# Kernel optimization log

Measured on AMD Instinct MI355X. Metric: run time of the kernel, lower is better.

## Reference

```python
import jax, jax.numpy as jnp
import numpy as np

B, C, H, W, D, V = 1, 32, 128, 160, 48, 3


def _make_proj_matrices():
    # K @ [R|t] per view, small rotations/baselines so warps land mostly in-bounds
    K = np.array([[400.0, 0.0, 80.0], [0.0, 400.0, 64.0], [0.0, 0.0, 1.0]])
    mats = []
    for v in range(V):
        a = 0.04 * v
        R = np.array([[np.cos(a), 0.0, np.sin(a)], [0.0, 1.0, 0.0], [-np.sin(a), 0.0, np.cos(a)]])
        t = np.array([120.0 * v, 0.0, 0.0])  # baseline in mm, consistent with depth ~425..935
        P = np.eye(4)
        P[:3, :3] = K @ R
        P[:3, 3] = K @ t
        mats.append(P)
    return jnp.asarray(np.stack(mats)[None], dtype=jnp.float32)  # [1,V,4,4]


def setup_inputs() -> dict:
    key = jax.random.key(0)
    k0, k1, k2, kw = jax.random.split(key, 4)
    feat0 = jax.random.normal(k0, (B, C, H, W), jnp.float32)
    feat1 = jax.random.normal(k1, (B, C, H, W), jnp.float32)
    feat2 = jax.random.normal(k2, (B, C, H, W), jnp.float32)
    depth_values = jnp.broadcast_to(
        jnp.linspace(425.0, 935.0, D, dtype=jnp.float32)[None], (B, D))
    w_reg = jax.random.normal(kw, (1, C, 3, 3, 3), jnp.float32) * 0.05
    b_reg = jnp.zeros((1,), jnp.float32)
    return dict(feat0=feat0, feat1=feat1, feat2=feat2,
                proj_matrices=_make_proj_matrices(),
                depth_values=depth_values, w_reg=w_reg, b_reg=b_reg,
                num_depth=D)


def _bilinear_sample(fea, gx, gy):
    # fea: [C,H,W]; gx,gy: [N] pixel coords (align_corners=True convention),
    # zero padding outside image (matches F.grid_sample padding_mode='zeros').
    h, w = fea.shape[1], fea.shape[2]
    x0 = jnp.floor(gx)
    y0 = jnp.floor(gy)
    wx = gx - x0
    wy = gy - y0

    def corner(xi, yi, wgt):
        valid = ((xi >= 0) & (xi <= w - 1) & (yi >= 0) & (yi <= h - 1)).astype(fea.dtype)
        xc = jnp.clip(xi, 0, w - 1).astype(jnp.int32)
        yc = jnp.clip(yi, 0, h - 1).astype(jnp.int32)
        return fea[:, yc, xc] * (wgt * valid)[None]  # [C,N]

    return (corner(x0, y0, (1 - wx) * (1 - wy)) +
            corner(x0 + 1, y0, wx * (1 - wy)) +
            corner(x0, y0 + 1, (1 - wx) * wy) +
            corner(x0 + 1, y0 + 1, wx * wy))


def homo_warping(src_fea, src_proj, ref_proj, depth_values):
    # src_fea [B,C,H,W], projs [B,4,4], depth_values [B,D] -> [B,C,D,H,W]
    b, c, h, w = src_fea.shape
    d = depth_values.shape[1]
    proj = src_proj @ jnp.linalg.inv(ref_proj)
    rot = proj[:, :3, :3]           # [B,3,3]
    trans = proj[:, :3, 3]          # [B,3]
    yy, xx = jnp.meshgrid(jnp.arange(h, dtype=src_fea.dtype),
                          jnp.arange(w, dtype=src_fea.dtype), indexing='ij')
    xyz = jnp.stack([xx.ravel(), yy.ravel(), jnp.ones(h * w, src_fea.dtype)], 0)  # [3,HW]
    rot_xyz = jnp.einsum('bij,jn->bin', rot, xyz)                                  # [B,3,HW]
    p = rot_xyz[:, :, None, :] * depth_values[:, None, :, None] + trans[:, :, None, None]  # [B,3,D,HW]
    z = p[:, 2]
    gx = (p[:, 0] / z).reshape(b, -1)  # [B, D*HW]
    gy = (p[:, 1] / z).reshape(b, -1)
    warped = jax.vmap(_bilinear_sample)(src_fea, gx, gy)  # [B,C,D*HW]
    return warped.reshape(b, c, d, h, w)


def reference(feat0, feat1, feat2, proj_matrices, depth_values, w_reg, b_reg, num_depth):
    features = [feat0, feat1, feat2]
    projs = [proj_matrices[:, v] for v in range(proj_matrices.shape[1])]
    ref_fea, ref_proj = features[0], projs[0]
    num_views = len(features)
    b, c, h, w = ref_fea.shape

    ref_volume = jnp.broadcast_to(ref_fea[:, :, None], (b, c, num_depth, h, w))
    volume_sum = ref_volume
    volume_sq_sum = ref_volume ** 2
    for src_fea, src_proj in zip(features[1:], projs[1:]):
        wv = homo_warping(src_fea, src_proj, ref_proj, depth_values)
        volume_sum = volume_sum + wv
        volume_sq_sum = volume_sq_sum + wv * wv

    volume_variance = volume_sq_sum / num_views - (volume_sum / num_views) ** 2

    # cost_regularization stand-in: 3D conv C -> 1, SAME padding, then squeeze channel
    cost = jax.lax.conv_general_dilated(
        volume_variance, w_reg, window_strides=(1, 1, 1), padding='SAME',
        dimension_numbers=('NCDHW', 'OIDHW', 'NCDHW'))
    cost = cost[:, 0] + b_reg[0]            # [B,D,H,W]

    prob_volume = jax.nn.softmax(cost, axis=1)
    depth = jnp.sum(prob_volume * depth_values[:, :, None, None], axis=1)  # [B,H,W]
    photometric_confidence = jnp.max(prob_volume, axis=1)                   # [B,H,W]
    return depth, photometric_confidence
```

## Files before the change

kernel.cpp:

```cpp
#include <hip/hip_runtime.h>
#include <hip/hip_fp16.h>
#include <math.h>

#define Cc 32
#define Hc 128
#define Wc 160
#define Dc 48
#define HWc (Hc*Wc)
#define TS 16
#define HALO (TS+2)
#define NPOS (HALO*HALO)
#define DCHUNK 4
#define NCHUNK (Dc/DCHUNK)
#define VSTR4 5
#define NPASS 6


typedef _Float16 h2 __attribute__((ext_vector_type(2)));

static __device__ __forceinline__ float hdot2(h2 a, h2 b, float acc) {
#if __has_builtin(__builtin_amdgcn_fdot2)
    return __builtin_amdgcn_fdot2(a, b, acc, false);
#else
    return fmaf((float)a.y, (float)b.y, fmaf((float)a.x, (float)b.x, acc));
#endif
}

union F4H { float4 f; __half2 h[4]; h2 d[4]; };
union PackCW { __half2 h[4]; float4 f; };

__global__ void k_pre(const float* __restrict__ f0, const float* __restrict__ f1,
                      const float* __restrict__ f2, const float* __restrict__ proj,
                      const float* __restrict__ wreg,
                      _Float16* __restrict__ o0, _Float16* __restrict__ o1, _Float16* __restrict__ o2,
                      float* __restrict__ wsproj, _Float16* __restrict__ w2h,
                      float* __restrict__ costvol) {
    const int tid = threadIdx.x;
    const int p = blockIdx.x * 256 + tid;
    if (blockIdx.y == 3) {
        if (p < HWc) {
#pragma unroll
            for (int d = 0; d < Dc; d++) costvol[d * HWc + p] = 0.f;
        }
        return;
    }
    if (p < HWc) {
        const float* f = (blockIdx.y == 0) ? f0 : (blockIdx.y == 1) ? f1 : f2;
        _Float16*    o = (blockIdx.y == 0) ? o0 : (blockIdx.y == 1) ? o1 : o2;
        float v[Cc];
#pragma unroll
        for (int c = 0; c < Cc; c++) v[c] = f[c * HWc + p];
        union { __half2 h[16]; float4 f4[4]; } rec;
#pragma unroll
        for (int c = 0; c < 16; c++) rec.h[c] = __floats2half2_rn(v[2 * c], v[2 * c + 1]);
        float4* o4 = (float4*)(o + (size_t)p * Cc);
#pragma unroll
        for (int j = 0; j < 4; j++) o4[j] = rec.f4[j];
    }
    if (blockIdx.x == 0 && blockIdx.y == 0) {
        for (int i = tid; i < 9 * 3 * Cc; i += 256) {
            int ch = i & 31;
            int t  = i >> 5;
            int kd = t % 3;
            int khkw = t / 3;
            w2h[i] = (_Float16)wreg[ch * 27 + kd * 9 + khkw];
        }
        if (tid == 0) {
            float a[4][8];
            for (int i = 0; i < 4; i++)
                for (int j = 0; j < 4; j++) {
                    a[i][j]     = proj[i * 4 + j];
                    a[i][j + 4] = (i == j) ? 1.f : 0.f;
                }
            for (int col = 0; col < 4; col++) {
                int piv = col; float best = fabsf(a[col][col]);
                for (int r = col + 1; r < 4; r++) {
                    float v = fabsf(a[r][col]);
                    if (v > best) { best = v; piv = r; }
                }
                if (piv != col)
                    for (int j = 0; j < 8; j++) { float t = a[col][j]; a[col][j] = a[piv][j]; a[piv][j] = t; }
                float inv = 1.f / a[col][col];
                for (int j = 0; j < 8; j++) a[col][j] *= inv;
                for (int r = 0; r < 4; r++) if (r != col) {
                    float f = a[r][col];
                    for (int j = 0; j < 8; j++) a[r][j] -= f * a[col][j];
                }
            }
            for (int v = 1; v < 3; v++) {
                const float* P = proj + v * 16;
                float M[3][4];
                for (int i = 0; i < 3; i++)
                    for (int j = 0; j < 4; j++) {
                        float s = 0.f;
                        for (int k = 0; k < 4; k++) s += P[i * 4 + k] * a[k][4 + j];
                        M[i][j] = s;
                    }
                float* o = wsproj + (v - 1) * 12;
                o[0] = M[0][0]; o[1] = M[0][1]; o[2] = M[0][2];
                o[3] = M[1][0]; o[4] = M[1][1]; o[5] = M[1][2];
                o[6] = M[2][0]; o[7] = M[2][1]; o[8] = M[2][2];
                o[9] = M[0][3]; o[10] = M[1][3]; o[11] = M[2][3];
            }
        }
    }
}

__global__ __launch_bounds__(256, 2) void k_cost(
    const _Float16* __restrict__ fT0, const _Float16* __restrict__ fT1,
    const _Float16* __restrict__ fT2, const float* __restrict__ dvals,
    const float4* __restrict__ w2h4, const float* __restrict__ wsproj,
    float* __restrict__ costvol)
{
    __shared__ float4 var_l[NPOS * VSTR4];
    __shared__ float4 parW[NPOS];
    __shared__ float4 parI[NPOS];
    __shared__ float projl[24];

    const int tid = threadIdx.x;
    if (tid < 24) projl[tid] = wsproj[tid];
    __syncthreads();

    const int tileX = blockIdx.x;
    const int tileY = blockIdx.y;
    const int d0    = blockIdx.z * DCHUNK;
    const int tx = tid & 15, ty = tid >> 4;
    const int baseH = tileY * TS - 1, baseW = tileX * TS - 1;

    const int posq = tid >> 2;
    const int cc   = tid & 3;

    const float4* fT0_4 = (const float4*)fT0;
    const float4* fT1_4 = (const float4*)fT1;
    const float4* fT2_4 = (const float4*)fT2;

    float rAx[2][2], rAy[2][2], rAz[2][2];
    float trn[2][3];
#pragma unroll
    for (int v = 0; v < 2; v++) {
        trn[v][0] = projl[v * 12 + 9];
        trn[v][1] = projl[v * 12 + 10];
        trn[v][2] = projl[v * 12 + 11];
    }
    int amask = 0;
#pragma unroll
    for (int s = 0; s < 2; s++) {
        int p = tid + s * 256;
        bool act = p < NPOS;
        int pp = act ? p : 0;
        int py = pp / HALO, px = pp % HALO;
        int hyi = baseH + py, hxi = baseW + px;
        bool ok = act && hyi >= 0 && hyi < Hc && hxi >= 0 && hxi < Wc;
        if (ok) amask |= (1 << s);
        float hx = (float)hxi, hy = (float)hyi;
#pragma unroll
        for (int v = 0; v < 2; v++) {
            const float* R = projl + v * 12;
            rAx[s][v] = fmaf(R[0], hx, fmaf(R[1], hy, R[2]));
            rAy[s][v] = fmaf(R[3], hx, fmaf(R[4], hy, R[5]));
            rAz[s][v] = fmaf(R[6], hx, fmaf(R[7], hy, R[8]));
        }
    }

    int    bmask = 0;
    float4 rfv[NPASS];
#pragma unroll
    for (int s = 0; s < NPASS; s++) {
        int p = posq + s * 64;
        bool act = p < NPOS;
        int pp = act ? p : 0;
        int py = pp / HALO, px = pp % HALO;
        int hyi = baseH + py, hxi = baseW + px;
        bool ok = act && hyi >= 0 && hyi < Hc && hxi >= 0 && hxi < Wc;
        if (ok) bmask |= (1 << s);
        rfv[s] = ok ? fT0_4[(hyi * Wc + hxi) * 4 + cc] : make_float4(0.f, 0.f, 0.f, 0.f);
    }

    float cost[DCHUNK];
#pragma unroll
    for (int i = 0; i < DCHUNK; i++) cost[i] = 0.f;
    float bndLo = 0.f, bndHi = 0.f;

    const int cb = ty * HALO + tx;

    auto phaseA = [&](int dpn) {
        const float depthN = dvals[dpn];
#pragma unroll
        for (int s = 0; s < 2; s++) {
            int p = tid + s * 256;
            if (p >= NPOS) break;
            if (!((amask >> s) & 1)) continue;
            float cw[2][4]; unsigned int pk[4];
#pragma unroll
            for (int v = 0; v < 2; v++) {
                float X = fmaf(rAx[s][v], depthN, trn[v][0]);
                float Y = fmaf(rAy[s][v], depthN, trn[v][1]);
                float Z = fmaf(rAz[s][v], depthN, trn[v][2]);
                float iz = 1.f / Z;
                float gx = X * iz, gy = Y * iz;
                float x0f = floorf(gx), y0f = floorf(gy);
                float wx = gx - x0f, wy = gy - y0f;
                int x0 = (int)x0f, y0 = (int)y0f;
                bool vx0 = (x0 >= 0) & (x0 <= Wc - 1);
                bool vx1 = (x0 + 1 >= 0) & (x0 + 1 <= Wc - 1);
                bool vy0 = (y0 >= 0) & (y0 <= Hc - 1);
                bool vy1 = (y0 + 1 >= 0) & (y0 + 1 <= Hc - 1);
                int xc0 = min(max(x0, 0), Wc - 1), xc1 = min(max(x0 + 1, 0), Wc - 1);
                int yc0 = min(max(y0, 0), Hc - 1), yc1 = min(max(y0 + 1, 0), Hc - 1);
                float ax = 1.f - wx, ay = 1.f - wy;
                cw[v][0] = (vx0 && vy0) ? ax * ay : 0.f;
                cw[v][1] = (vx1 && vy0) ? wx * ay : 0.f;
                cw[v][2] = (vx0 && vy1) ? ax * wy : 0.f;
                cw[v][3] = (vx1 && vy1) ? wx * wy : 0.f;
                unsigned int i0 = (unsigned int)(yc0 * Wc + xc0);
                unsigned int i1 = (unsigned int)(yc0 * Wc + xc1);
                unsigned int i2 = (unsigned int)(yc1 * Wc + xc0);
                unsigned int i3 = (unsigned int)(yc1 * Wc + xc1);
                pk[v * 2 + 0] = i0 | (i1 << 16);
                pk[v * 2 + 1] = i2 | (i3 << 16);
            }
            PackCW pc;
            pc.h[0] = __floats2half2_rn(cw[0][0], cw[0][1]);
            pc.h[1] = __floats2half2_rn(cw[0][2], cw[0][3]);
            pc.h[2] = __floats2half2_rn(cw[1][0], cw[1][1]);
            pc.h[3] = __floats2half2_rn(cw[1][2], cw[1][3]);
            parW[p] = pc.f;
            parI[p] = make_float4(__uint_as_float(pk[0]), __uint_as_float(pk[1]),
                                  __uint_as_float(pk[2]), __uint_as_float(pk[3]));
        }
    };

    const int dpFirst = d0;
    const int dpLast  = d0 + DCHUNK - 1;

    phaseA(dpFirst);
    __syncthreads();

    const __half2 kT3 = __float2half2_rn(1.f / 3.f);
    const __half2 kN9 = __float2half2_rn(-1.f / 9.f);

    for (int dp = dpFirst; dp <= dpLast; dp++) {
#pragma unroll
        for (int s = 0; s < NPASS; s++) {
            int p = posq + s * 64;
            if (p >= NPOS) continue;
            const int vaddr = p * VSTR4 + cc;
            if (!((bmask >> s) & 1)) {
                var_l[vaddr] = make_float4(0.f, 0.f, 0.f, 0.f);
                continue;
            }
            PackCW pc; pc.f = parW[p];
            float4 pkf = parI[p];
            __half2 c0a = __low2half2(pc.h[0]), c0b = __high2half2(pc.h[0]);
            __half2 c0c = __low2half2(pc.h[1]), c0d = __high2half2(pc.h[1]);
            __half2 c1a = __low2half2(pc.h[2]), c1b = __high2half2(pc.h[2]);
            __half2 c1c = __low2half2(pc.h[3]), c1d = __high2half2(pc.h[3]);
            unsigned int u0 = __float_as_uint(pkf.x), u1 = __float_as_uint(pkf.y);
            unsigned int u2 = __float_as_uint(pkf.z), u3 = __float_as_uint(pkf.w);
            int i00 = u0 & 0xffff, i01 = u0 >> 16, i02 = u1 & 0xffff, i03 = u1 >> 16;
            int i10 = u2 & 0xffff, i11 = u2 >> 16, i12 = u3 & 0xffff, i13 = u3 >> 16;
            F4H rf; rf.f = rfv[s];
            F4H t00, t01, t10, t11, u00v, u01v, u10v, u11v, vo;
            t00.f = fT1_4[i00 * 4 + cc];
            t01.f = fT1_4[i01 * 4 + cc];
            t10.f = fT1_4[i02 * 4 + cc];
            t11.f = fT1_4[i03 * 4 + cc];
            u00v.f = fT2_4[i10 * 4 + cc];
            u01v.f = fT2_4[i11 * 4 + cc];
            u10v.f = fT2_4[i12 * 4 + cc];
            u11v.f = fT2_4[i13 * 4 + cc];
#pragma unroll
            for (int j = 0; j < 4; j++) {
                __half2 a1 = __hfma2(c0a, t00.h[j], __hfma2(c0b, t01.h[j],
                             __hfma2(c0c, t10.h[j], __hmul2(c0d, t11.h[j]))));
                __half2 a2 = __hfma2(c1a, u00v.h[j], __hfma2(c1b, u01v.h[j],
                             __hfma2(c1c, u10v.h[j], __hmul2(c1d, u11v.h[j]))));
                __half2 r  = rf.h[j];
                __half2 sm = __hadd2(r, __hadd2(a1, a2));
                __half2 sq = __hfma2(r, r, __hfma2(a1, a1, __hmul2(a2, a2)));
                vo.h[j] = __hfma2(__hmul2(sm, sm), kN9, __hmul2(sq, kT3));
            }
            var_l[vaddr] = vo.f;
        }
        __syncthreads();

        if (dp < dpLast) phaseA(dp + 1);

        float a0 = 0.f, a1 = 0.f, a2 = 0.f;
#pragma unroll
        for (int k = 0; k < 9; k++) {
            const int vp = (cb + (k / 3) * HALO + (k % 3)) * VSTR4;
            F4H va[4];
#pragma unroll
            for (int j = 0; j < 4; j++) va[j].f = var_l[vp + j];
            const int wb = k * 12;
#pragma unroll
            for (int j = 0; j < 4; j++) {
                F4H w0, w1, w2v;
                w0.f  = w2h4[wb + 0 + j];
                w1.f  = w2h4[wb + 4 + j];
                w2v.f = w2h4[wb + 8 + j];
#pragma unroll
                for (int i = 0; i < 4; i++) {
                    a0 = hdot2(va[j].d[i], w0.d[i], a0);
                    a1 = hdot2(va[j].d[i], w1.d[i], a1);
                    a2 = hdot2(va[j].d[i], w2v.d[i], a2);
                }
            }
        }
        cost[dp - d0] += a1;
        int r0 = dp + 1 - d0;
        if (r0 < DCHUNK) cost[r0] += a0; else bndHi = a0;
        int r2 = dp - 1 - d0;
        if (r2 >= 0) cost[r2] += a2; else bndLo = a2;
        __syncthreads();
    }

    const int h = tileY * TS + ty, w = tileX * TS + tx;
    float* base = costvol + h * Wc + w;
#pragma unroll
    for (int i = 0; i < DCHUNK; i++)
        atomicAdd(base + (size_t)(d0 + i) * HWc, cost[i]);
    if (d0 > 0)            atomicAdd(base + (size_t)(d0 - 1) * HWc, bndLo);
    if (d0 + DCHUNK < Dc)  atomicAdd(base + (size_t)(d0 + DCHUNK) * HWc, bndHi);
}

__global__ void k_softmax(const float* __restrict__ costvol, const float* __restrict__ dvals,
                          const float* __restrict__ breg, float* __restrict__ out)
{
    const int px = blockIdx.x * 256 + threadIdx.x;
    if (px >= HWc) return;
    const float bias = breg[0];
    float c[Dc];
    float m = -1e30f;
#pragma unroll
    for (int d = 0; d < Dc; d++) {
        c[d] = costvol[d * HWc + px] + bias;
        m = fmaxf(m, c[d]);
    }
    float se = 0.f, sed = 0.f, me = 0.f;
#pragma unroll
    for (int d = 0; d < Dc; d++) {
        float e = __expf(c[d] - m);
        se += e;
        sed = fmaf(e, dvals[d], sed);
        me = fmaxf(me, e);
    }
    float inv = 1.f / se;
    out[px]       = sed * inv;
    out[HWc + px] = me * inv;
}

extern "C" void kernel_launch(void* const* d_in, const int* in_sizes, int n_in,
                              void* d_out, int out_size, void* d_ws, size_t ws_size,
                              hipStream_t stream) {
    const float* f0    = (const float*)d_in[0];
    const float* f1    = (const float*)d_in[1];
    const float* f2    = (const float*)d_in[2];
    const float* proj  = (const float*)d_in[3];
    const float* dvals = (const float*)d_in[4];
    const float* wreg  = (const float*)d_in[5];
    const float* breg  = (const float*)d_in[6];

    float* ws      = (float*)d_ws;
    float* wsproj  = ws;
    _Float16* w2h  = (_Float16*)(ws + 32);
    _Float16* fT0h = (_Float16*)(ws + 32 + 432);
    _Float16* fT1h = fT0h + (size_t)HWc * Cc;
    _Float16* fT2h = fT1h + (size_t)HWc * Cc;
    float* costvol = (float*)(fT2h + (size_t)HWc * Cc);

    k_pre<<<dim3((HWc + 255) / 256, 4), 256, 0, stream>>>(f0, f1, f2, proj, wreg,
                                                          fT0h, fT1h, fT2h, wsproj, w2h,
                                                          costvol);

    dim3 grid(Wc / TS, Hc / TS, NCHUNK);
    k_cost<<<grid, 256, 0, stream>>>(fT0h, fT1h, fT2h, dvals, (const float4*)w2h,
                                     wsproj, costvol);

    k_softmax<<<(HWc + 255) / 256, 256, 0, stream>>>(costvol, dvals, breg, (float*)d_out);
}
```

Measured before the change: 138.3 us.

## Compute 3D cost convolution with MFMA 16x16x32 f16 instead of scalar dot2

Replaces the per-thread fdot2 loop over 9 spatial taps and 3 depth taps with MFMA matrix instructions. Each wave handles 4 output rows of the 16x16 tile, treating 16 pixels × 32 channels as the A operand and the per-tap weights (3 depth outputs padded to 16 columns) as B fragments preloaded into registers. Results are scattered straight to the global cost volume with per-depth-step atomicAdds instead of accumulating in registers over the chunk. This trades many scalar dot instructions for matrix ops, but adds many more global atomics and wastes 13 of 16 MFMA output columns.

```diff
diff --git a/kernel.cpp b/kernel.cpp
--- a/kernel.cpp
+++ b/kernel.cpp
@@ -16,18 +16,12 @@
 #define NPASS 6
 
 
-typedef _Float16 h2 __attribute__((ext_vector_type(2)));
-
-static __device__ __forceinline__ float hdot2(h2 a, h2 b, float acc) {
-#if __has_builtin(__builtin_amdgcn_fdot2)
-    return __builtin_amdgcn_fdot2(a, b, acc, false);
-#else
-    return fmaf((float)a.y, (float)b.y, fmaf((float)a.x, (float)b.x, acc));
-#endif
-}
-
-union F4H { float4 f; __half2 h[4]; h2 d[4]; };
+typedef _Float16 h8v __attribute__((ext_vector_type(8)));
+typedef float f32x4 __attribute__((ext_vector_type(4)));
+
+union F4H { float4 f; __half2 h[4]; };
 union PackCW { __half2 h[4]; float4 f; };
+union AF { float4 f; h8v h; };
 
 __global__ void k_pre(const float* __restrict__ f0, const float* __restrict__ f1,
                       const float* __restrict__ f2, const float* __restrict__ proj,
@@ -124,15 +118,29 @@
     const int tileX = blockIdx.x;
     const int tileY = blockIdx.y;
     const int d0    = blockIdx.z * DCHUNK;
-    const int tx = tid & 15, ty = tid >> 4;
     const int baseH = tileY * TS - 1, baseW = tileX * TS - 1;
 
     const int posq = tid >> 2;
     const int cc   = tid & 3;
+
+    const int wid  = tid >> 6;
+    const int lane = tid & 63;
+    const int lrow = lane & 15;
+    const int lsel = lane >> 4;
 
     const float4* fT0_4 = (const float4*)fT0;
     const float4* fT1_4 = (const float4*)fT1;
     const float4* fT2_4 = (const float4*)fT2;
+
+    h8v bfr[9];
+    {
+        const int kdc = (lrow < 3) ? lrow : 0;
+#pragma unroll
+        for (int t = 0; t < 9; t++) {
+            AF u; u.f = w2h4[(t * 3 + kdc) * 4 + lsel];
+            bfr[t] = u.h;
+        }
+    }
 
     float rAx[2][2], rAy[2][2], rAz[2][2];
     float trn[2][3];
@@ -175,13 +183,6 @@
         if (ok) bmask |= (1 << s);
         rfv[s] = ok ? fT0_4[(hyi * Wc + hxi) * 4 + cc] : make_float4(0.f, 0.f, 0.f, 0.f);
     }
-
-    float cost[DCHUNK];
-#pragma unroll
-    for (int i = 0; i < DCHUNK; i++) cost[i] = 0.f;
-    float bndLo = 0.f, bndHi = 0.f;
-
-    const int cb = ty * HALO + tx;
 
     auto phaseA = [&](int dpn) {
         const float depthN = dvals[dpn];
@@ -286,43 +287,28 @@
 
         if (dp < dpLast) phaseA(dp + 1);
 
-        float a0 = 0.f, a1 = 0.f, a2 = 0.f;
-#pragma unroll
-        for (int k = 0; k < 9; k++) {
-            const int vp = (cb + (k / 3) * HALO + (k % 3)) * VSTR4;
-            F4H va[4];
-#pragma unroll
-            for (int j = 0; j < 4; j++) va[j].f = var_l[vp + j];
-            const int wb = k * 12;
-#pragma unroll
-            for (int j = 0; j < 4; j++) {
-                F4H w0, w1, w2v;
-                w0.f  = w2h4[wb + 0 + j];
-                w1.f  = w2h4[wb + 4 + j];
-                w2v.f = w2h4[wb + 8 + j];
-#pragma unroll
-                for (int i = 0; i < 4; i++) {
-                    a0 = hdot2(va[j].d[i], w0.d[i], a0);
-                    a1 = hdot2(va[j].d[i], w1.d[i], a1);
-                    a2 = hdot2(va[j].d[i], w2v.d[i], a2);
+#pragma unroll
+        for (int g = 0; g < 4; g++) {
+            const int R = (wid << 2) + g;
+            f32x4 acc = {0.f, 0.f, 0.f, 0.f};
+#pragma unroll
+            for (int t = 0; t < 9; t++) {
+                const int dy = t / 3, dx = t % 3;
+                AF a; a.f = var_l[((R + dy) * HALO + dx + lrow) * VSTR4 + lsel];
+                acc = __builtin_amdgcn_mfma_f32_16x16x32_f16(a.h, bfr[t], acc, 0, 0, 0);
+            }
+            if (lrow < 3) {
+                const int sIdx = dp + 1 - lrow;
+                if (sIdx >= 0 && sIdx < Dc) {
+                    float* dst = costvol + (size_t)sIdx * HWc
+                               + (tileY * TS + R) * Wc + tileX * TS + (lsel << 2);
+#pragma unroll
+                    for (int i = 0; i < 4; i++) atomicAdd(dst + i, acc[i]);
                 }
             }
         }
-        cost[dp - d0] += a1;
-        int r0 = dp + 1 - d0;
-        if (r0 < DCHUNK) cost[r0] += a0; else bndHi = a0;
-        int r2 = dp - 1 - d0;
-        if (r2 >= 0) cost[r2] += a2; else bndLo = a2;
         __syncthreads();
     }
-
-    const int h = tileY * TS + ty, w = tileX * TS + tx;
-    float* base = costvol + h * Wc + w;
-#pragma unroll
-    for (int i = 0; i < DCHUNK; i++)
-        atomicAdd(base + (size_t)(d0 + i) * HWc, cost[i]);
-    if (d0 > 0)            atomicAdd(base + (size_t)(d0 - 1) * HWc, bndLo);
-    if (d0 + DCHUNK < Dc)  atomicAdd(base + (size_t)(d0 + DCHUNK) * HWc, bndHi);
 }
 
 __global__ void k_softmax(const float* __restrict__ costvol, const float* __restrict__ dvals,
```

Result: faster. 133.5 us (-3.5%).
